# Performance work log

Measured on AMD Instinct MI355X. Metric: run time of the kernel, lower is better.

The kernel has to match this reference:

```python
import jax, jax.numpy as jnp
import numpy as np

B, S, C, D, H, FF, DEPTH, T, N = 8, 1024, 2, 512, 8, 2048, 6, 64, 16
HD = D // H
EPS = 1e-5


def _ln(x, w, b):
    m = jnp.mean(x, axis=-1, keepdims=True)
    v = jnp.mean(jnp.square(x - m), axis=-1, keepdims=True)
    return (x - m) * jax.lax.rsqrt(v + EPS) * w + b


def setup_inputs() -> dict:
    key = jax.random.key(0)
    ks = jax.random.split(key, 24)
    w = lambda k, shape: (jax.random.normal(k, shape, jnp.float32) * 0.02)
    return {
        "src": jax.random.normal(ks[0], (B, S, D), jnp.float32),
        "ctx_emb": jax.random.normal(ks[1], (B, C, D), jnp.float32),
        "times": jax.random.randint(ks[2], (B, S), 0, T),
        "spaces": jax.random.randint(ks[3], (B, S), 0, N),
        "pad_mask": jnp.zeros((B, S + C), bool),
        "time_emb": w(ks[4], (T, D)),
        "space_emb": w(ks[5], (N, D)),
        "Wqkv": w(ks[6], (DEPTH, 3 * D, D)),
        "bqkv": jnp.zeros((DEPTH, 3 * D), jnp.float32),
        "Wo": w(ks[7], (DEPTH, D, D)),
        "bo": jnp.zeros((DEPTH, D), jnp.float32),
        "ln1_w": jnp.ones((DEPTH, D), jnp.float32),
        "ln1_b": jnp.zeros((DEPTH, D), jnp.float32),
        "W1": w(ks[8], (DEPTH, FF, D)),
        "b1": jnp.zeros((DEPTH, FF), jnp.float32),
        "W2": w(ks[9], (DEPTH, D, FF)),
        "b2": jnp.zeros((DEPTH, D), jnp.float32),
        "ln2_w": jnp.ones((DEPTH, D), jnp.float32),
        "ln2_b": jnp.zeros((DEPTH, D), jnp.float32),
    }


def _forward(src, ctx_emb, times, spaces, pad_mask, time_emb, space_emb,
             Wqkv, bqkv, Wo, bo, ln1_w, ln1_b, W1, b1, W2, b2, ln2_w, ln2_b):
    NEG = -jnp.inf
    # learned time/space positional embeddings, then append context tokens
    x = src + time_emb[times] + space_emb[spaces]          # [B,S,D]
    x = jnp.concatenate([x, ctx_emb], axis=1)              # [B,L,D], L=S+C
    # per-batch additive float mask: causal-in-time over src tokens,
    # ctx tokens attendable by everyone, ctx rows attend only to ctx.
    cond = times[:, :, None] >= times[:, None, :]          # [B,S,S]
    m = jnp.where(cond, 0.0, NEG)
    m = jnp.pad(m, ((0, 0), (0, C), (0, 0)), constant_values=NEG)  # ctx rows
    m = jnp.pad(m, ((0, 0), (0, 0), (0, C)), constant_values=0.0)  # ctx cols
    m = m + jnp.where(pad_mask[:, None, :], NEG, 0.0)      # key padding
    m = m[:, None]                                         # [B,1,L,L]

    scale = 1.0 / np.sqrt(HD)
    Bc, L, _ = x.shape
    for i in range(DEPTH):
        # --- self-attention (post-norm encoder layer) ---
        qkv = x @ Wqkv[i].T + bqkv[i]                      # [B,L,3D]
        q, k, v = jnp.split(qkv, 3, axis=-1)
        split = lambda t: t.reshape(Bc, L, H, HD).transpose(0, 2, 1, 3)
        q, k, v = split(q), split(k), split(v)             # [B,H,L,HD]
        scores = jnp.einsum('bhqd,bhkd->bhqk', q, k) * scale + m
        p = jax.nn.softmax(scores, axis=-1)
        a = jnp.einsum('bhqk,bhkd->bhqd', p, v)
        a = a.transpose(0, 2, 1, 3).reshape(Bc, L, D)
        a = a @ Wo[i].T + bo[i]
        x = _ln(x + a, ln1_w[i], ln1_b[i])
        # --- feed-forward ---
        h = jax.nn.gelu(x @ W1[i].T + b1[i], approximate=False)
        h = h @ W2[i].T + b2[i]
        x = _ln(x + h, ln2_w[i], ln2_b[i])
    return x[:, :S]                                        # drop ctx tokens


def reference(src, ctx_emb, times, spaces, pad_mask, time_emb, space_emb,
              Wqkv, bqkv, Wo, bo, ln1_w, ln1_b, W1, b1, W2, b2, ln2_w, ln2_b):
    return _forward(src, ctx_emb, times, spaces, pad_mask, time_emb, space_emb,
                    Wqkv, bqkv, Wo, bo, ln1_w, ln1_b, W1, b1, W2, b2, ln2_w, ln2_b)
```

## Files before the change

### kernel.cpp

```cpp
#include <hip/hip_runtime.h>
#include <hip/hip_bf16.h>

#define BB 8
#define SS 1024
#define CC 2
#define DD 512
#define NH 8
#define FF2 2048
#define NL 6
#define LL 1026
#define HD 64
#define MROWS 8208
#define MP 8320
#define KVPAD 1152

typedef __attribute__((ext_vector_type(8))) short bf16x8;
typedef __attribute__((ext_vector_type(4))) float f32x4;

typedef __attribute__((address_space(3))) void lds_void;
typedef __attribute__((address_space(1))) void g_void;

__device__ __forceinline__ void gll16(const void* g, void* l) {
  __builtin_amdgcn_global_load_lds((const g_void*)g, (lds_void*)l, 16, 0, 0);
}

__global__ __launch_bounds__(256) void cvt_bf16_k(const float* __restrict__ in,
                                                  __hip_bfloat16* __restrict__ out) {
  int i = (blockIdx.x * 256 + threadIdx.x) * 4;
  float4 v = *(const float4*)&in[i];
  out[i + 0] = __float2bfloat16(v.x);
  out[i + 1] = __float2bfloat16(v.y);
  out[i + 2] = __float2bfloat16(v.z);
  out[i + 3] = __float2bfloat16(v.w);
}

__global__ __launch_bounds__(256) void embed_k(const float* __restrict__ src,
    const float* __restrict__ ctx, const int* __restrict__ times,
    const int* __restrict__ spaces, const float* __restrict__ te,
    const float* __restrict__ se, float* __restrict__ x,
    __hip_bfloat16* __restrict__ xb) {
  int row = blockIdx.x;
  int b = row / LL, l = row % LL;
  int c = threadIdx.x * 2;
  float y0, y1;
  if (l < SS) {
    const float* sp = src + ((size_t)(b * SS + l)) * DD + c;
    int tt = times[b * SS + l], ssp = spaces[b * SS + l];
    y0 = sp[0] + te[tt * DD + c] + se[ssp * DD + c];
    y1 = sp[1] + te[tt * DD + c + 1] + se[ssp * DD + c + 1];
  } else {
    const float* cp = ctx + ((size_t)(b * CC + (l - SS))) * DD + c;
    y0 = cp[0]; y1 = cp[1];
  }
  size_t o = (size_t)row * DD + c;
  x[o] = y0; x[o + 1] = y1;
  xb[o] = __float2bfloat16(y0); xb[o + 1] = __float2bfloat16(y1);
}

template <int EPI>
__global__ __launch_bounds__(256) void gemm_bt(const __hip_bfloat16* __restrict__ A,
    const __hip_bfloat16* __restrict__ W, const float* __restrict__ bias,
    void* __restrict__ outp, int K, int N) {
  __shared__ __hip_bfloat16 As[64 * 64];
  __shared__ __hip_bfloat16 Bs[128 * 64];
  const int tid = threadIdx.x;
  const int lane = tid & 63, wv = tid >> 6;
  const int ny = N >> 7;
  const int nwg = gridDim.x;
  int qq = nwg >> 3, rr = nwg & 7;
  int xcd = blockIdx.x & 7, loc = blockIdx.x >> 3;
  int slot = (xcd < rr ? xcd * (qq + 1) : rr * (qq + 1) + (xcd - rr) * qq) + loc;
  const int m0 = (slot / ny) * 64, n0 = (slot % ny) * 128;
  const int r0 = lane & 15, kq = lane >> 4;
  f32x4 acc[4][2] = {};
  for (int k0 = 0; k0 < K; k0 += 64) {
    __syncthreads();
#pragma unroll
    for (int c = 0; c < 6; ++c) {
      int ch = c * 256 + tid;
      if (ch < 512) {
        int row = ch >> 3, cp = ch & 7;
        gll16(A + (size_t)(m0 + row) * K + k0 + cp * 8, (char*)As + ch * 16);
      } else {
        int bi = ch - 512;
        int row = bi >> 3, cp = bi & 7;
        gll16(W + (size_t)(n0 + row) * K + k0 + cp * 8, (char*)Bs + bi * 16);
      }
    }
    __syncthreads();
#pragma unroll
    for (int kk = 0; kk < 64; kk += 32) {
      bf16x8 af[4], bfr[2];
#pragma unroll
      for (int m = 0; m < 4; ++m)
        af[m] = *(const bf16x8*)&As[(m * 16 + r0) * 64 + kk + kq * 8];
#pragma unroll
      for (int n = 0; n < 2; ++n)
        bfr[n] = *(const bf16x8*)&Bs[(wv * 32 + n * 16 + r0) * 64 + kk + kq * 8];
#pragma unroll
      for (int m = 0; m < 4; ++m)
#pragma unroll
        for (int n = 0; n < 2; ++n)
          acc[m][n] = __builtin_amdgcn_mfma_f32_16x16x32_bf16(af[m], bfr[n], acc[m][n], 0, 0, 0);
    }
  }
#pragma unroll
  for (int m = 0; m < 4; ++m) {
    int grow_base = m0 + m * 16 + kq * 4;
#pragma unroll
    for (int n = 0; n < 2; ++n) {
      int gcol = n0 + wv * 32 + n * 16 + r0;
      float bv = (EPI == 0) ? 0.f : bias[gcol];
#pragma unroll
      for (int j = 0; j < 4; ++j) {
        int grow = grow_base + j;
        float v = acc[m][n][j] + bv;
        ((__hip_bfloat16*)outp)[(size_t)grow * N + gcol] = __float2bfloat16(v);
      }
    }
  }
}

template <int EPI>
__global__ __launch_bounds__(512) void gemm_bt2(const __hip_bfloat16* __restrict__ A,
    const __hip_bfloat16* __restrict__ W, const float* __restrict__ bias,
    void* __restrict__ outp, int K, int N) {
  __shared__ __hip_bfloat16 As[128 * 64];
  __shared__ __hip_bfloat16 Bs[256 * 64];
  const int tid = threadIdx.x;
  const int lane = tid & 63, wv = tid >> 6;
  const int ny = N >> 8;
  const int nwg = gridDim.x;
  int qq = nwg >> 3, rr = nwg & 7;
  int xcd = blockIdx.x & 7, loc = blockIdx.x >> 3;
  int slot = (xcd < rr ? xcd * (qq + 1) : rr * (qq + 1) + (xcd - rr) * qq) + loc;
  const int m0 = (slot / ny) * 128, n0 = (slot % ny) * 256;
  const int wr = wv >> 2, wc = wv & 3;
  const int r0 = lane & 15, kq = lane >> 4;
  f32x4 acc[4][4] = {};
  for (int k0 = 0; k0 < K; k0 += 64) {
    __syncthreads();
#pragma unroll
    for (int c = 0; c < 6; ++c) {
      int ch = c * 512 + tid;
      if (ch < 1024) {
        int row = ch >> 3, cp = ch & 7;
        gll16(A + (size_t)(m0 + row) * K + k0 + cp * 8, (char*)As + ch * 16);
      } else {
        int bi = ch - 1024;
        int row = bi >> 3, cp = bi & 7;
        gll16(W + (size_t)(n0 + row) * K + k0 + cp * 8, (char*)Bs + bi * 16);
      }
    }
    __syncthreads();
#pragma unroll
    for (int kk = 0; kk < 64; kk += 32) {
      bf16x8 af[4], bfr[4];
#pragma unroll
      for (int m = 0; m < 4; ++m)
        af[m] = *(const bf16x8*)&As[(wr * 64 + m * 16 + r0) * 64 + kk + kq * 8];
#pragma unroll
      for (int n = 0; n < 4; ++n)
        bfr[n] = *(const bf16x8*)&Bs[(wc * 64 + n * 16 + r0) * 64 + kk + kq * 8];
#pragma unroll
      for (int m = 0; m < 4; ++m)
#pragma unroll
        for (int n = 0; n < 4; ++n)
          acc[m][n] = __builtin_amdgcn_mfma_f32_16x16x32_bf16(af[m], bfr[n], acc[m][n], 0, 0, 0);
    }
  }
#pragma unroll
  for (int m = 0; m < 4; ++m) {
    int grow_base = m0 + wr * 64 + m * 16 + kq * 4;
#pragma unroll
    for (int n = 0; n < 4; ++n) {
      int gcol = n0 + wc * 64 + n * 16 + r0;
      float bv = bias[gcol];
#pragma unroll
      for (int j = 0; j < 4; ++j) {
        int grow = grow_base + j;
        float v = acc[m][n][j] + bv;
        if (EPI == 2) v = 0.5f * v * (1.f + erff(v * 0.70710678f));
        ((__hip_bfloat16*)outp)[(size_t)grow * N + gcol] = __float2bfloat16(v);
      }
    }
  }
}

__global__ __launch_bounds__(256) void vtrans_k(const __hip_bfloat16* __restrict__ qkv,
                                                __hip_bfloat16* __restrict__ vt) {
  __shared__ __hip_bfloat16 tile[64][72];
  int bh = blockIdx.y;
  int b = bh >> 3, hh = bh & 7;
  int l0 = blockIdx.x * 64;
  int t = threadIdx.x;
  int lr = t >> 2, part = t & 3;
  int l = l0 + lr;
  if (l < LL) {
    const __hip_bfloat16* p = qkv + (size_t)(b * LL + l) * 1536 + 1024 + hh * 64 + part * 16;
    *(uint4*)&tile[lr][part * 16] = *(const uint4*)p;
    *(uint4*)&tile[lr][part * 16 + 8] = *(const uint4*)(p + 8);
  } else {
    uint4 z = make_uint4(0, 0, 0, 0);
    *(uint4*)&tile[lr][part * 16] = z;
    *(uint4*)&tile[lr][part * 16 + 8] = z;
  }
  __syncthreads();
  int d = t >> 2, kp = t & 3;
  __hip_bfloat16 vals[16];
#pragma unroll
  for (int i = 0; i < 16; ++i) vals[i] = tile[kp * 16 + i][d];
  __hip_bfloat16* o = vt + ((size_t)(bh * 64 + d)) * KVPAD + l0 + kp * 16;
  *(uint4*)o = *(uint4*)&vals[0];
  *(uint4*)(o + 8) = *(uint4*)&vals[8];
}

#define TK_CTX (-2000000000)
#define TQ_CTX (-1000000000)
#define TK_INV (2000000000)

__global__ __launch_bounds__(256) void attn_k(const __hip_bfloat16* __restrict__ qkv,
    const __hip_bfloat16* __restrict__ vt, const int* __restrict__ times,
    __hip_bfloat16* __restrict__ aout) {
  __shared__ __hip_bfloat16 Kl[128 * 64];
  __shared__ __hip_bfloat16 Vl[64 * 128];
  __shared__ __hip_bfloat16 Pl[4][16 * 128];
  const int tid = threadIdx.x, lane = tid & 63, wv = tid >> 6;
  const int r0 = lane & 15, kq = lane >> 4;
  int i = blockIdx.x;
  int xcd = i & 7, slot = i >> 3;
  int bhl = slot / 17;
  int qb = slot - bhl * 17;
  int bh = xcd * 8 + bhl;
  int b = bh >> 3, hh = bh & 7;
  char* plbase = (char*)&Pl[wv][0];

  const int qbase = qb * 64 + wv * 16;
  int qr = qbase + r0;
  if (qr > LL - 1) qr = LL - 1;
  const __hip_bfloat16* qp = qkv + (size_t)(b * LL + qr) * 1536 + hh * 64;
  bf16x8 qa0 = *(const bf16x8*)(qp + kq * 8);
  bf16x8 qa1 = *(const bf16x8*)(qp + 32 + kq * 8);
  int tq[4];
#pragma unroll
  for (int j = 0; j < 4; ++j) {
    int r = qbase + kq * 4 + j;
    tq[j] = (r < SS) ? times[b * SS + r] : TQ_CTX;
  }
  float m_run[4] = {-1e30f, -1e30f, -1e30f, -1e30f};
  float l_run[4] = {0.f, 0.f, 0.f, 0.f};
  f32x4 O[4] = {};
  const float scale = 0.125f;

  for (int kc = 0; kc < 9; ++kc) {
    __syncthreads();
#pragma unroll
    for (int c = 0; c < 4; ++c) {
      int chb = c * 256 + wv * 64;
      int ch = chb + lane;
      {
        int trow = ch >> 3, cp = ch & 7;
        int krow = kc * 128 + trow;
        if (krow > LL - 1) krow = LL - 1;
        int scp = cp ^ (trow & 7);
        gll16(qkv + (size_t)(b * LL + krow) * 1536 + 512 + hh * 64 + scp * 8,
              (char*)Kl + chb * 16);
      }
      {
        int d = ch >> 4, kp = ch & 15;
        int skp = kp ^ (d & 7);
        gll16(vt + ((size_t)(bh * 64 + d)) * KVPAD + kc * 128 + skp * 8,
              (char*)Vl + chb * 16);
      }
    }
    __syncthreads();
    f32x4 s[8] = {};
#pragma unroll
    for (int n = 0; n < 8; ++n) {
      int row = n * 16 + r0;
      bf16x8 kb0 = *(const bf16x8*)&Kl[row * 64 + ((kq ^ (row & 7)) * 8)];
      bf16x8 kb1 = *(const bf16x8*)&Kl[row * 64 + (((4 + kq) ^ (row & 7)) * 8)];
      s[n] = __builtin_amdgcn_mfma_f32_16x16x32_bf16(qa0, kb0, s[n], 0, 0, 0);
      s[n] = __builtin_amdgcn_mfma_f32_16x16x32_bf16(qa1, kb1, s[n], 0, 0, 0);
    }
    int tkn[8];
#pragma unroll
    for (int n = 0; n < 8; ++n) {
      int k = kc * 128 + 16 * n + r0;
      tkn[n] = (k < SS) ? times[b * SS + k] : ((k < LL) ? TK_CTX : TK_INV);
    }
    float mch[4] = {-1e30f, -1e30f, -1e30f, -1e30f};
#pragma unroll
    for (int n = 0; n < 8; ++n)
#pragma unroll
      for (int j = 0; j < 4; ++j) {
        float sv = (tq[j] >= tkn[n]) ? s[n][j] * scale : -1e30f;
        s[n][j] = sv;
        mch[j] = fmaxf(mch[j], sv);
      }
#pragma unroll
    for (int j = 0; j < 4; ++j) {
#pragma unroll
      for (int off = 1; off < 16; off <<= 1)
        mch[j] = fmaxf(mch[j], __shfl_xor(mch[j], off, 64));
    }
    float fac[4], psum[4];
#pragma unroll
    for (int j = 0; j < 4; ++j) {
      float mn = fmaxf(m_run[j], mch[j]);
      fac[j] = __expf(m_run[j] - mn);
      m_run[j] = mn;
      psum[j] = 0.f;
    }
#pragma unroll
    for (int n = 0; n < 8; ++n)
#pragma unroll
      for (int j = 0; j < 4; ++j) {
        float p = __expf(s[n][j] - m_run[j]);
        s[n][j] = p;
        psum[j] += p;
      }
#pragma unroll
    for (int j = 0; j < 4; ++j) {
#pragma unroll
      for (int off = 1; off < 16; off <<= 1)
        psum[j] += __shfl_xor(psum[j], off, 64);
      l_run[j] = l_run[j] * fac[j] + psum[j];
    }
#pragma unroll
    for (int n = 0; n < 4; ++n)
#pragma unroll
      for (int j = 0; j < 4; ++j) O[n][j] *= fac[j];
#pragma unroll
    for (int n = 0; n < 8; ++n)
#pragma unroll
      for (int j = 0; j < 4; ++j) {
        int q = kq * 4 + j;
        int byte = ((r0 + 16 * n) * 2) ^ ((q & 7) << 4);
        *(__hip_bfloat16*)(plbase + q * 256 + byte) = __float2bfloat16(s[n][j]);
      }
#pragma unroll
    for (int c = 0; c < 4; ++c) {
      int rbyte = (c * 64 + kq * 16) ^ ((r0 & 7) << 4);
      bf16x8 pa = *(const bf16x8*)(plbase + r0 * 256 + rbyte);
#pragma unroll
      for (int n = 0; n < 4; ++n) {
        int d = n * 16 + r0;
        int chv = (c * 4 + kq) ^ (r0 & 7);
        bf16x8 vb = *(const bf16x8*)&Vl[d * 128 + chv * 8];
        O[n] = __builtin_amdgcn_mfma_f32_16x16x32_bf16(pa, vb, O[n], 0, 0, 0);
      }
    }
  }
#pragma unroll
  for (int j = 0; j < 4; ++j) {
    int orow = qbase + kq * 4 + j;
    if (orow < LL) {
      float inv = 1.f / l_run[j];
#pragma unroll
      for (int n = 0; n < 4; ++n)
        aout[(size_t)(b * LL + orow) * DD + hh * 64 + n * 16 + r0] =
            __float2bfloat16(O[n][j] * inv);
    }
  }
}

__global__ __launch_bounds__(256) void ln_fuse_k(float* __restrict__ x,
    const __hip_bfloat16* __restrict__ tmp, const float* __restrict__ gb,
    const float* __restrict__ w, const float* __restrict__ bias,
    __hip_bfloat16* __restrict__ xb, float* __restrict__ fout) {
  const int row = blockIdx.x;
  const int tid = threadIdx.x;
  size_t o = (size_t)row * DD + tid * 2;
  float2 v = *(const float2*)&x[o];
  const __hip_bfloat16* tp = tmp + o;
  float t0 = __bfloat162float(tp[0]);
  float t1 = __bfloat162float(tp[1]);
  float a0 = v.x + gb[tid * 2] + t0, a1 = v.y + gb[tid * 2 + 1] + t1;
  float s = a0 + a1, ss = a0 * a0 + a1 * a1;
#pragma unroll
  for (int off = 1; off < 64; off <<= 1) {
    s += __shfl_xor(s, off, 64);
    ss += __shfl_xor(ss, off, 64);
  }
  __shared__ float red[8];
  const int wv = tid >> 6, lane = tid & 63;
  if (lane == 0) { red[wv] = s; red[4 + wv] = ss; }
  __syncthreads();
  s = red[0] + red[1] + red[2] + red[3];
  ss = red[4] + red[5] + red[6] + red[7];
  float mean = s * (1.f / 512.f);
  float var = ss * (1.f / 512.f) - mean * mean;
  if (var < 0.f) var = 0.f;
  float rs = rsqrtf(var + 1e-5f);
  float w0 = w[tid * 2], w1 = w[tid * 2 + 1];
  float b0 = bias[tid * 2], b1 = bias[tid * 2 + 1];
  float y0 = (a0 - mean) * rs * w0 + b0;
  float y1 = (a1 - mean) * rs * w1 + b1;
  x[o] = y0; x[o + 1] = y1;
  xb[o] = __float2bfloat16(y0); xb[o + 1] = __float2bfloat16(y1);
  if (fout != nullptr) {
    int b = row / LL, l = row - b * LL;
    if (l < SS) {
      float* fp = fout + ((size_t)(b * SS + l)) * DD + tid * 2;
      fp[0] = y0; fp[1] = y1;
    }
  }
}

extern "C" void kernel_launch(void* const* d_in, const int* in_sizes, int n_in,
                              void* d_out, int out_size, void* d_ws, size_t ws_size,
                              hipStream_t stream) {
  (void)in_sizes; (void)n_in; (void)out_size; (void)ws_size;
  const float* src    = (const float*)d_in[0];
  const float* ctx    = (const float*)d_in[1];
  const int*   times  = (const int*)d_in[2];
  const int*   spaces = (const int*)d_in[3];
  const float* te     = (const float*)d_in[5];
  const float* se     = (const float*)d_in[6];
  const float* Wqkv   = (const float*)d_in[7];
  const float* bqkv   = (const float*)d_in[8];
  const float* Wo     = (const float*)d_in[9];
  const float* bo     = (const float*)d_in[10];
  const float* ln1w   = (const float*)d_in[11];
  const float* ln1b   = (const float*)d_in[12];
  const float* W1     = (const float*)d_in[13];
  const float* b1     = (const float*)d_in[14];
  const float* W2     = (const float*)d_in[15];
  const float* b2     = (const float*)d_in[16];
  const float* ln2w   = (const float*)d_in[17];
  const float* ln2b   = (const float*)d_in[18];

  char* ws = (char*)d_ws;
  size_t off = 0;
  auto alloc = [&](size_t bytes) {
    size_t o = off;
    off += (bytes + 255) & ~(size_t)255;
    return o;
  };
  float* x            = (float*)(ws + alloc((size_t)MP * DD * 4));
  __hip_bfloat16* xb  = (__hip_bfloat16*)(ws + alloc((size_t)MP * DD * 2));
  __hip_bfloat16* qkv = (__hip_bfloat16*)(ws + alloc((size_t)MP * 3 * DD * 2));
  __hip_bfloat16* abf = (__hip_bfloat16*)(ws + alloc((size_t)MP * DD * 2));
  __hip_bfloat16* hbf = (__hip_bfloat16*)(ws + alloc((size_t)MP * FF2 * 2));
  __hip_bfloat16* tmp = (__hip_bfloat16*)(ws + alloc((size_t)MP * DD * 2));
  __hip_bfloat16* vt  = (__hip_bfloat16*)(ws + alloc((size_t)BB * NH * HD * KVPAD * 2));
  __hip_bfloat16* wqb = (__hip_bfloat16*)(ws + alloc((size_t)NL * 3 * DD * DD * 2));
  __hip_bfloat16* wob = (__hip_bfloat16*)(ws + alloc((size_t)NL * DD * DD * 2));
  __hip_bfloat16* w1b = (__hip_bfloat16*)(ws + alloc((size_t)NL * FF2 * DD * 2));
  __hip_bfloat16* w2b = (__hip_bfloat16*)(ws + alloc((size_t)NL * DD * FF2 * 2));

  cvt_bf16_k<<<(NL * 3 * DD * DD) / 1024, 256, 0, stream>>>(Wqkv, wqb);
  cvt_bf16_k<<<(NL * DD * DD) / 1024, 256, 0, stream>>>(Wo, wob);
  cvt_bf16_k<<<(NL * FF2 * DD) / 1024, 256, 0, stream>>>(W1, w1b);
  cvt_bf16_k<<<(NL * DD * FF2) / 1024, 256, 0, stream>>>(W2, w2b);

  embed_k<<<MROWS, 256, 0, stream>>>(src, ctx, times, spaces, te, se, x, xb);

  for (int i = 0; i < NL; ++i) {
    gemm_bt2<1><<<65 * 6, 512, 0, stream>>>(
        xb, wqb + (size_t)i * 3 * DD * DD, bqkv + i * 3 * DD, qkv, DD, 3 * DD);
    vtrans_k<<<dim3(17, BB * NH), 256, 0, stream>>>(qkv, vt);
    attn_k<<<1088, 256, 0, stream>>>(qkv, vt, times, abf);
    gemm_bt<0><<<130 * 4, 256, 0, stream>>>(
        abf, wob + (size_t)i * DD * DD, nullptr, tmp, DD, DD);
    ln_fuse_k<<<MROWS, 256, 0, stream>>>(x, tmp, bo + i * DD,
                                         ln1w + i * DD, ln1b + i * DD, xb, nullptr);
    gemm_bt2<2><<<65 * 8, 512, 0, stream>>>(
        xb, w1b + (size_t)i * FF2 * DD, b1 + i * FF2, hbf, DD, FF2);
    gemm_bt<0><<<130 * 4, 256, 0, stream>>>(
        hbf, w2b + (size_t)i * DD * FF2, nullptr, tmp, FF2, DD);
    ln_fuse_k<<<MROWS, 256, 0, stream>>>(x, tmp, b2 + i * DD,
                                         ln2w + i * DD, ln2b + i * DD, xb,
                                         (i == NL - 1) ? (float*)d_out : nullptr);
  }
}
```

Before: 1.418 ms.

## Double-buffer LDS tiles in GEMM kernels to overlap global loads with MFMA

Both GEMM kernels now keep two LDS buffers with a K-step of 32, and issue the next tile's global-to-LDS loads before computing on the current one. Explicit vmcnt waits and barriers replace the load-then-sync-then-compute loop, so memory latency is meant to hide behind MFMA work. The cost is twice as many loop iterations and barriers per K, and smaller per-step compute that may not fully cover load latency.

```diff
diff --git a/kernel.cpp b/kernel.cpp
--- a/kernel.cpp
+++ b/kernel.cpp
@@ -61,8 +61,8 @@
 __global__ __launch_bounds__(256) void gemm_bt(const __hip_bfloat16* __restrict__ A,
     const __hip_bfloat16* __restrict__ W, const float* __restrict__ bias,
     void* __restrict__ outp, int K, int N) {
-  __shared__ __hip_bfloat16 As[64 * 64];
-  __shared__ __hip_bfloat16 Bs[128 * 64];
+  __shared__ __hip_bfloat16 As[2][64 * 32];
+  __shared__ __hip_bfloat16 Bs[2][128 * 32];
   const int tid = threadIdx.x;
   const int lane = tid & 63, wv = tid >> 6;
   const int ny = N >> 7;
@@ -73,37 +73,54 @@
   const int m0 = (slot / ny) * 64, n0 = (slot % ny) * 128;
   const int r0 = lane & 15, kq = lane >> 4;
   f32x4 acc[4][2] = {};
-  for (int k0 = 0; k0 < K; k0 += 64) {
-    __syncthreads();
-#pragma unroll
-    for (int c = 0; c < 6; ++c) {
+
+  auto STAGE = [&](int nb, int t) {
+    int k0 = t * 32;
+#pragma unroll
+    for (int c = 0; c < 3; ++c) {
       int ch = c * 256 + tid;
-      if (ch < 512) {
-        int row = ch >> 3, cp = ch & 7;
-        gll16(A + (size_t)(m0 + row) * K + k0 + cp * 8, (char*)As + ch * 16);
+      if (ch < 256) {
+        int row = ch >> 2, cp = ch & 3;
+        gll16(A + (size_t)(m0 + row) * K + k0 + cp * 8, (char*)&As[nb][0] + ch * 16);
       } else {
-        int bi = ch - 512;
-        int row = bi >> 3, cp = bi & 7;
-        gll16(W + (size_t)(n0 + row) * K + k0 + cp * 8, (char*)Bs + bi * 16);
-      }
-    }
-    __syncthreads();
-#pragma unroll
-    for (int kk = 0; kk < 64; kk += 32) {
-      bf16x8 af[4], bfr[2];
-#pragma unroll
-      for (int m = 0; m < 4; ++m)
-        af[m] = *(const bf16x8*)&As[(m * 16 + r0) * 64 + kk + kq * 8];
+        int bi = ch - 256;
+        int row = bi >> 2, cp = bi & 3;
+        gll16(W + (size_t)(n0 + row) * K + k0 + cp * 8, (char*)&Bs[nb][0] + bi * 16);
+      }
+    }
+  };
+  auto COMPUTE = [&](int nb) {
+    bf16x8 af[4], bfr[2];
+#pragma unroll
+    for (int m = 0; m < 4; ++m)
+      af[m] = *(const bf16x8*)&As[nb][(m * 16 + r0) * 32 + kq * 8];
+#pragma unroll
+    for (int n = 0; n < 2; ++n)
+      bfr[n] = *(const bf16x8*)&Bs[nb][(wv * 32 + n * 16 + r0) * 32 + kq * 8];
+#pragma unroll
+    for (int m = 0; m < 4; ++m)
 #pragma unroll
       for (int n = 0; n < 2; ++n)
-        bfr[n] = *(const bf16x8*)&Bs[(wv * 32 + n * 16 + r0) * 64 + kk + kq * 8];
-#pragma unroll
-      for (int m = 0; m < 4; ++m)
-#pragma unroll
-        for (int n = 0; n < 2; ++n)
-          acc[m][n] = __builtin_amdgcn_mfma_f32_16x16x32_bf16(af[m], bfr[n], acc[m][n], 0, 0, 0);
-    }
-  }
+        acc[m][n] = __builtin_amdgcn_mfma_f32_16x16x32_bf16(af[m], bfr[n], acc[m][n], 0, 0, 0);
+  };
+
+  const int nt = K >> 5;
+  STAGE(0, 0);
+  asm volatile("s_waitcnt vmcnt(0)" ::: "memory");
+  __builtin_amdgcn_s_barrier();
+  for (int t = 0; t < nt - 1; ++t) {
+    STAGE((t + 1) & 1, t + 1);
+    asm volatile("s_waitcnt vmcnt(3)" ::: "memory");
+    __builtin_amdgcn_s_barrier();
+    __builtin_amdgcn_sched_barrier(0);
+    COMPUTE(t & 1);
+    __builtin_amdgcn_s_barrier();
+  }
+  asm volatile("s_waitcnt vmcnt(0)" ::: "memory");
+  __builtin_amdgcn_s_barrier();
+  __builtin_amdgcn_sched_barrier(0);
+  COMPUTE((nt - 1) & 1);
+
 #pragma unroll
   for (int m = 0; m < 4; ++m) {
     int grow_base = m0 + m * 16 + kq * 4;
@@ -125,8 +142,8 @@
 __global__ __launch_bounds__(512) void gemm_bt2(const __hip_bfloat16* __restrict__ A,
     const __hip_bfloat16* __restrict__ W, const float* __restrict__ bias,
     void* __restrict__ outp, int K, int N) {
-  __shared__ __hip_bfloat16 As[128 * 64];
-  __shared__ __hip_bfloat16 Bs[256 * 64];
+  __shared__ __hip_bfloat16 As[2][128 * 32];
+  __shared__ __hip_bfloat16 Bs[2][256 * 32];
   const int tid = threadIdx.x;
   const int lane = tid & 63, wv = tid >> 6;
   const int ny = N >> 8;
@@ -138,37 +155,54 @@
   const int wr = wv >> 2, wc = wv & 3;
   const int r0 = lane & 15, kq = lane >> 4;
   f32x4 acc[4][4] = {};
-  for (int k0 = 0; k0 < K; k0 += 64) {
-    __syncthreads();
-#pragma unroll
-    for (int c = 0; c < 6; ++c) {
+
+  auto STAGE = [&](int nb, int t) {
+    int k0 = t * 32;
+#pragma unroll
+    for (int c = 0; c < 3; ++c) {
       int ch = c * 512 + tid;
-      if (ch < 1024) {
-        int row = ch >> 3, cp = ch & 7;
-        gll16(A + (size_t)(m0 + row) * K + k0 + cp * 8, (char*)As + ch * 16);
+      if (ch < 512) {
+        int row = ch >> 2, cp = ch & 3;
+        gll16(A + (size_t)(m0 + row) * K + k0 + cp * 8, (char*)&As[nb][0] + ch * 16);
       } else {
-        int bi = ch - 1024;
-        int row = bi >> 3, cp = bi & 7;
-        gll16(W + (size_t)(n0 + row) * K + k0 + cp * 8, (char*)Bs + bi * 16);
-      }
-    }
-    __syncthreads();
-#pragma unroll
-    for (int kk = 0; kk < 64; kk += 32) {
-      bf16x8 af[4], bfr[4];
-#pragma unroll
-      for (int m = 0; m < 4; ++m)
-        af[m] = *(const bf16x8*)&As[(wr * 64 + m * 16 + r0) * 64 + kk + kq * 8];
+        int bi = ch - 512;
+        int row = bi >> 2, cp = bi & 3;
+        gll16(W + (size_t)(n0 + row) * K + k0 + cp * 8, (char*)&Bs[nb][0] + bi * 16);
+      }
+    }
+  };
+  auto COMPUTE = [&](int nb) {
+    bf16x8 af[4], bfr[4];
+#pragma unroll
+    for (int m = 0; m < 4; ++m)
+      af[m] = *(const bf16x8*)&As[nb][(wr * 64 + m * 16 + r0) * 32 + kq * 8];
+#pragma unroll
+    for (int n = 0; n < 4; ++n)
+      bfr[n] = *(const bf16x8*)&Bs[nb][(wc * 64 + n * 16 + r0) * 32 + kq * 8];
+#pragma unroll
+    for (int m = 0; m < 4; ++m)
 #pragma unroll
       for (int n = 0; n < 4; ++n)
-        bfr[n] = *(const bf16x8*)&Bs[(wc * 64 + n * 16 + r0) * 64 + kk + kq * 8];
-#pragma unroll
-      for (int m = 0; m < 4; ++m)
-#pragma unroll
-        for (int n = 0; n < 4; ++n)
-          acc[m][n] = __builtin_amdgcn_mfma_f32_16x16x32_bf16(af[m], bfr[n], acc[m][n], 0, 0, 0);
-    }
-  }
+        acc[m][n] = __builtin_amdgcn_mfma_f32_16x16x32_bf16(af[m], bfr[n], acc[m][n], 0, 0, 0);
+  };
+
+  const int nt = K >> 5;
+  STAGE(0, 0);
+  asm volatile("s_waitcnt vmcnt(0)" ::: "memory");
+  __builtin_amdgcn_s_barrier();
+  for (int t = 0; t < nt - 1; ++t) {
+    STAGE((t + 1) & 1, t + 1);
+    asm volatile("s_waitcnt vmcnt(3)" ::: "memory");
+    __builtin_amdgcn_s_barrier();
+    __builtin_amdgcn_sched_barrier(0);
+    COMPUTE(t & 1);
+    __builtin_amdgcn_s_barrier();
+  }
+  asm volatile("s_waitcnt vmcnt(0)" ::: "memory");
+  __builtin_amdgcn_s_barrier();
+  __builtin_amdgcn_sched_barrier(0);
+  COMPUTE((nt - 1) & 1);
+
 #pragma unroll
   for (int m = 0; m < 4; ++m) {
     int grow_base = m0 + wr * 64 + m * 16 + kq * 4;
```

Result: faster. 1.335 ms, median of 3 (-5.9%).
